# Performance work log

Measured on AMD Instinct MI355X. Metric: run time of the kernel, lower is better.

## Reference

```python
import jax, jax.numpy as jnp
import numpy as np

D_MODEL = 768
NUM_HEADS = 12
HEAD_DIM = D_MODEL // NUM_HEADS
ROPE_THETA = 10000.0
MAX_SEQ_LEN = 2048
BATCH = 2
SEQ = 2048


def _rope_tables():
    # powers = arange(0, d_k, 2)/d_k ; freqs = theta**-powers ; angles = t outer freqs
    powers = jnp.arange(0, HEAD_DIM, 2, dtype=jnp.float32) / HEAD_DIM
    freqs = 1.0 / (ROPE_THETA ** powers)                      # [d_k/2]
    t = jnp.arange(MAX_SEQ_LEN, dtype=jnp.float32)
    angles = t[:, None] * freqs[None, :]                      # [max_seq_len, d_k/2]
    return jnp.cos(angles), jnp.sin(angles)


def _apply_rope(x, cos, sin, pos):
    # x: [b, h, s, d], pos: [b, s]; interleaved even/odd pairing
    c = cos[pos][:, None]          # [b, 1, s, d/2]
    s = sin[pos][:, None]
    x_even = x[..., 0::2]
    x_odd = x[..., 1::2]
    new_even = x_even * c - x_odd * s
    new_odd = x_even * s + x_odd * c
    # re-interleave: (..., f, 2) -> (..., 2f)
    return jnp.stack([new_even, new_odd], axis=-1).reshape(x.shape)


def setup_inputs() -> dict:
    key = jax.random.key(0)
    k1, k2, k3 = jax.random.split(key, 3)
    x = jax.random.normal(k1, (BATCH, SEQ, D_MODEL), dtype=jnp.float32)
    token_positions = jnp.broadcast_to(jnp.arange(SEQ, dtype=jnp.int32), (BATCH, SEQ))
    sigma_qkv = (2.0 / (D_MODEL + 3 * D_MODEL)) ** 0.5
    sigma_o = (2.0 / (D_MODEL + D_MODEL)) ** 0.5
    W_qkv = jax.random.normal(k2, (3 * D_MODEL, D_MODEL), dtype=jnp.float32) * sigma_qkv
    W_o = jax.random.normal(k3, (D_MODEL, D_MODEL), dtype=jnp.float32) * sigma_o
    return {"x": x, "token_positions": token_positions, "W_qkv": W_qkv, "W_o": W_o}


def reference(x, token_positions, W_qkv, W_o):
    b, s, _ = x.shape
    cos, sin = _rope_tables()
    qkv = jnp.einsum('bsd,ed->bse', x, W_qkv)                 # [b, s, 3*d_model]
    qkv = qkv.reshape(b, s, 3, NUM_HEADS, HEAD_DIM)
    qkv = jnp.transpose(qkv, (2, 0, 3, 1, 4))                 # [3, b, h, s, hd]
    q, k, v = qkv[0], qkv[1], qkv[2]
    q = _apply_rope(q, cos, sin, token_positions)
    k = _apply_rope(k, cos, sin, token_positions)
    scores = jnp.einsum('bhqd,bhkd->bhqk', q, k) / (HEAD_DIM ** 0.5)
    causal = jnp.tril(jnp.ones((s, s), dtype=bool))
    scores = jnp.where(causal, scores, -jnp.inf)
    weights = jax.nn.softmax(scores, axis=-1)
    context = jnp.einsum('bhqk,bhkd->bhqd', weights, v)
    context = jnp.transpose(context, (0, 2, 1, 3)).reshape(b, s, D_MODEL)
    return jnp.einsum('bsd,ed->bse', context, W_o)
```

## Files before the change

kernel.cpp:

```cpp
#include <hip/hip_runtime.h>
#include <hip/hip_bf16.h>
#include <math.h>

#define SEQ 2048
#define DM 768
#define NH 12
#define HD 64
#define NB 2
#define NT (NB*SEQ)
#define E3 (3*DM)

using short4v = __attribute__((ext_vector_type(4))) short;
using short8v = __attribute__((ext_vector_type(8))) short;
using floatx4 = __attribute__((ext_vector_type(4))) float;
using int4v   = __attribute__((ext_vector_type(4))) int;

#if __has_builtin(__builtin_amdgcn_exp2f)
#define EXPFN(x) __builtin_amdgcn_exp2f(x)
#define QSCALE 0.1803368801111244f
#else
#define EXPFN(x) __expf(x)
#define QSCALE 0.125f
#endif

static __device__ __forceinline__ short bfb(float f) {
  union { __hip_bfloat16 h; short s; } u;
  u.h = __float2bfloat16(f);
  return u.s;
}

static __device__ __forceinline__ void gload_lds16(const __hip_bfloat16* g, __hip_bfloat16* lds) {
  __builtin_amdgcn_global_load_lds(
      (const __attribute__((address_space(1))) unsigned int*)g,
      (__attribute__((address_space(3))) unsigned int*)lds, 16, 0, 0);
}

static __device__ __forceinline__ int swzg(int row) {
  return (((row >> 3) & 3) + 2 * (row & 3)) & 7;
}

#define XN4 (NT * DM / 4)
#define WQN4 (E3 * DM / 4)
#define WON4 (DM * DM / 4)
#define CVT_N (XN4 + WQN4 + WON4)
__global__ void cvt3_rope(const float* __restrict__ x, const float* __restrict__ wq,
                          const float* __restrict__ wo,
                          __hip_bfloat16* __restrict__ xb, __hip_bfloat16* __restrict__ wqb,
                          __hip_bfloat16* __restrict__ wob, float2* __restrict__ rcs) {
  int i = blockIdx.x * blockDim.x + threadIdx.x;
  if (i >= CVT_N) {
    int idx = i - CVT_N;
    if (idx < SEQ * 32) {
      int pos = idx >> 5, j = idx & 31;
      float freq = __expf(-(float)j * (logf(10000.0f) / 32.0f));
      float ang = (float)pos * freq;
      rcs[idx] = make_float2(cosf(ang), sinf(ang));
    }
    return;
  }
  const float* src;
  __hip_bfloat16* dst;
  int k;
  if (i < XN4) { src = x; dst = xb; k = i; }
  else if (i < XN4 + WQN4) { src = wq; dst = wqb; k = i - XN4; }
  else { src = wo; dst = wob; k = i - XN4 - WQN4; }
  floatx4 v = ((const floatx4*)src)[k];
  short4v o;
  o[0] = bfb(v[0]); o[1] = bfb(v[1]); o[2] = bfb(v[2]); o[3] = bfb(v[3]);
  ((short4v*)dst)[k] = o;
}

__global__ __launch_bounds__(256) void qkv_gemm_rope(
    const __hip_bfloat16* __restrict__ Wq,
    const __hip_bfloat16* __restrict__ Xb,
    const int* __restrict__ tpos,
    const float2* __restrict__ rcs,
    __hip_bfloat16* __restrict__ Qb, __hip_bfloat16* __restrict__ Kb,
    __hip_bfloat16* __restrict__ Vt)
{
  __shared__ __align__(16) __hip_bfloat16 As[64 * 128];
  __shared__ __align__(16) __hip_bfloat16 Bs[128 * 128];
  const int tid = threadIdx.x;
  const int lane = tid & 63, w = tid >> 6;
  const int c = lane & 15, g = lane >> 4;
  const int wr = w >> 1, wc = w & 1;
  const int bid = blockIdx.x;
  const int xcd = bid & 7, i_ = bid >> 3;
  const int nb = xcd * 4 + (i_ & 3), mb = i_ >> 2;
  const int m0 = mb * 64, n0 = nb * 128;
  const int srow = tid >> 4, sslot = tid & 15;

  floatx4 acc[2][4] = {};
  for (int k0 = 0; k0 < DM; k0 += 128) {
#pragma unroll
    for (int j = 0; j < 4; ++j) {
      const int row = j * 16 + srow;
      const int gs = (sslot ^ (row & 15)) * 8;
      gload_lds16(Wq + (size_t)(m0 + row) * DM + k0 + gs, As + j * 2048 + w * 512);
    }
#pragma unroll
    for (int j = 0; j < 8; ++j) {
      const int row = j * 16 + srow;
      const int gs = (sslot ^ (row & 15)) * 8;
      gload_lds16(Xb + (size_t)(n0 + row) * DM + k0 + gs, Bs + j * 2048 + w * 512);
    }
    __syncthreads();
#pragma unroll
    for (int kk = 0; kk < 4; ++kk) {
      short8v a[2], b[4];
#pragma unroll
      for (int i = 0; i < 2; ++i) {
        const int row = wr * 32 + i * 16 + c;
        a[i] = *(const short8v*)&As[row * 128 + (((kk * 4 + g) ^ (row & 15)) * 8)];
      }
#pragma unroll
      for (int j = 0; j < 4; ++j) {
        const int row = wc * 64 + j * 16 + c;
        b[j] = *(const short8v*)&Bs[row * 128 + (((kk * 4 + g) ^ (row & 15)) * 8)];
      }
#pragma unroll
      for (int i = 0; i < 2; ++i)
#pragma unroll
        for (int j = 0; j < 4; ++j)
          acc[i][j] = __builtin_amdgcn_mfma_f32_16x16x32_bf16(a[i], b[j], acc[i][j], 0, 0, 0);
    }
    __syncthreads();
  }
#pragma unroll
  for (int i = 0; i < 2; ++i) {
    const int e0 = m0 + wr * 32 + i * 16 + 4 * g;
    const int jj = (e0 & 63) >> 1;
#pragma unroll
    for (int j = 0; j < 4; ++j) {
      const int t = n0 + wc * 64 + j * 16 + c;
      const int b_ = t >> 11, s = t & (SEQ - 1);
      float v0 = acc[i][j][0], v1 = acc[i][j][1], v2 = acc[i][j][2], v3 = acc[i][j][3];
      if (e0 < 2 * DM) {
        const int pos = tpos[t];
        const float2 cs0 = rcs[pos * 32 + jj];
        const float2 cs1 = rcs[pos * 32 + jj + 1];
        const float n0v = v0 * cs0.x - v1 * cs0.y, n1v = v0 * cs0.y + v1 * cs0.x;
        const float n2v = v2 * cs1.x - v3 * cs1.y, n3v = v2 * cs1.y + v3 * cs1.x;
        v0 = n0v; v1 = n1v; v2 = n2v; v3 = n3v;
      }
      if (e0 < DM) {
        const int h = e0 >> 6, d = e0 & 63;
        short4v pk;
        pk[0] = bfb(v0 * QSCALE); pk[1] = bfb(v1 * QSCALE);
        pk[2] = bfb(v2 * QSCALE); pk[3] = bfb(v3 * QSCALE);
        *(short4v*)&Qb[(((size_t)(b_ * NH + h) * SEQ) + s) * HD + d] = pk;
      } else if (e0 < 2 * DM) {
        const int e = e0 - DM, h = e >> 6, d = e & 63;
        short4v pk;
        pk[0] = bfb(v0); pk[1] = bfb(v1); pk[2] = bfb(v2); pk[3] = bfb(v3);
        *(short4v*)&Kb[(((size_t)(b_ * NH + h) * SEQ) + s) * HD + d] = pk;
      } else {
        const int e = e0 - 2 * DM, h = e >> 6, d = e & 63;
        const size_t base = ((size_t)(b_ * NH + h) * HD + d) * SEQ + s;
        Vt[base]           = __float2bfloat16(v0);
        Vt[base + SEQ]     = __float2bfloat16(v1);
        Vt[base + 2 * SEQ] = __float2bfloat16(v2);
        Vt[base + 3 * SEQ] = __float2bfloat16(v3);
      }
    }
  }
}

__global__ __launch_bounds__(512) void attn_fused(
    const __hip_bfloat16* __restrict__ Qb,
    const __hip_bfloat16* __restrict__ Kb,
    const __hip_bfloat16* __restrict__ Vt,
    __hip_bfloat16* __restrict__ Cx)
{
  __shared__ __align__(16) __hip_bfloat16 Ks[2][128 * 64];
  __shared__ __align__(16) __hip_bfloat16 Vs[2][64 * 128];
  const int tid = threadIdx.x;
  const int lane = tid & 63, w = tid >> 6;
  const int c = lane & 15, g = lane >> 4;
  const int bid = blockIdx.x;
  const int xcd = bid & 7, i_ = bid >> 3;
  const int bh = xcd + 8 * (i_ % 3);
  const int qG = 15 - i_ / 3;
  const int KBmax = qG;
  const __hip_bfloat16* Qh = Qb + (size_t)bh * SEQ * HD;
  const __hip_bfloat16* Kh = Kb + (size_t)bh * SEQ * HD;
  const __hip_bfloat16* Vh = Vt + (size_t)bh * HD * SEQ;
  const int q1 = qG * 128 + w * 16 + c;
  const int qt_w = 4 * qG + (w >> 1);
  const int qrl32 = (w & 1) * 16 + c;
  const short8v qf10 = *(const short8v*)&Qh[(size_t)q1 * HD + g * 8];
  const short8v qf11 = *(const short8v*)&Qh[(size_t)q1 * HD + 32 + g * 8];
  floatx4 o1[4] = {};
  float l1 = 0.0f;
  const int kr1 = 8 * (c >> 2) + (c & 3);

  const int ksr = w * 8 + (lane >> 3), kss = lane & 7;
  const int vsr = w * 4 + (lane >> 4), vss = lane & 15;

#define STAGE_KV(KB_, KSD, VSD)                                                       \
  do {                                                                               \
    _Pragma("unroll")                                                                \
    for (int j = 0; j < 2; ++j) {                                                    \
      const int kr = j * 64 + ksr;                                                   \
      gload_lds16(Kh + (size_t)((KB_) * 128 + kr) * HD + ((kss ^ swzg(kr)) * 8),     \
                  (KSD) + j * 4096 + w * 512);                                       \
      const int vr = j * 32 + vsr;                                                   \
      gload_lds16(Vh + (size_t)vr * SEQ + (KB_) * 128 + ((vss ^ (vr & 15)) * 8),     \
                  (VSD) + j * 4096 + w * 512);                                       \
    }                                                                                \
  } while (0)

  STAGE_KV(0, Ks[0], Vs[0]);
  __syncthreads();
  int cb = 0;
  for (int kb = 0; kb <= KBmax; ++kb) {
    if (kb < KBmax) STAGE_KV(kb + 1, Ks[cb ^ 1], Vs[cb ^ 1]);
    {
      const __hip_bfloat16* Kt = Ks[cb];
      const __hip_bfloat16* Vb = Vs[cb];
#pragma unroll
      for (int s = 0; s < 4; ++s) {
        const int kidx = 4 * kb + s;
        if (kidx <= qt_w) {
          const int r0 = s * 32 + kr1, r1 = r0 + 4;
          const int z0 = swzg(r0), z1 = swzg(r1);
          const short8v a00 = *(const short8v*)&Kt[r0 * 64 + ((g ^ z0) * 8)];
          const short8v a01 = *(const short8v*)&Kt[r0 * 64 + (((4 + g) ^ z0) * 8)];
          const short8v a10 = *(const short8v*)&Kt[r1 * 64 + ((g ^ z1) * 8)];
          const short8v a11 = *(const short8v*)&Kt[r1 * 64 + (((4 + g) ^ z1) * 8)];
          short8v vf[4];
#pragma unroll
          for (int f = 0; f < 4; ++f) {
            const int rv = f * 16 + c;
            vf[f] = *(const short8v*)&Vb[rv * 128 + (((s * 4 + g) ^ (rv & 15)) * 8)];
          }
          floatx4 s1a = {}, s1b = {};
          s1a = __builtin_amdgcn_mfma_f32_16x16x32_bf16(a00, qf10, s1a, 0, 0, 0);
          s1a = __builtin_amdgcn_mfma_f32_16x16x32_bf16(a01, qf11, s1a, 0, 0, 0);
          s1b = __builtin_amdgcn_mfma_f32_16x16x32_bf16(a10, qf10, s1b, 0, 0, 0);
          s1b = __builtin_amdgcn_mfma_f32_16x16x32_bf16(a11, qf11, s1b, 0, 0, 0);
          if (kidx == qt_w) {
#pragma unroll
            for (int r = 0; r < 4; ++r) {
              if (8 * g + r > qrl32) s1a[r] = -INFINITY;
              if (8 * g + r + 4 > qrl32) s1b[r] = -INFINITY;
            }
          }
          short8v pf1;
#pragma unroll
          for (int r = 0; r < 4; ++r) {
            float p;
            p = EXPFN(s1a[r]); l1 += p; pf1[r] = bfb(p);
            p = EXPFN(s1b[r]); l1 += p; pf1[r + 4] = bfb(p);
          }
          o1[0] = __builtin_amdgcn_mfma_f32_16x16x32_bf16(vf[0], pf1, o1[0], 0, 0, 0);
          o1[1] = __builtin_amdgcn_mfma_f32_16x16x32_bf16(vf[1], pf1, o1[1], 0, 0, 0);
          o1[2] = __builtin_amdgcn_mfma_f32_16x16x32_bf16(vf[2], pf1, o1[2], 0, 0, 0);
          o1[3] = __builtin_amdgcn_mfma_f32_16x16x32_bf16(vf[3], pf1, o1[3], 0, 0, 0);
        }
      }
    }
    __syncthreads();
    cb ^= 1;
  }
#undef STAGE_KV

  l1 += __shfl_xor(l1, 16); l1 += __shfl_xor(l1, 32);
  const float inv1 = 1.0f / l1;
  const int bb = bh / NH, h = bh - bb * NH;
  const size_t trow1 = ((size_t)bb * SEQ + q1) * DM + (size_t)h * HD;
#pragma unroll
  for (int f = 0; f < 4; ++f) {
    short4v pk1;
#pragma unroll
    for (int r = 0; r < 4; ++r) pk1[r] = bfb(o1[f][r] * inv1);
    *(short4v*)&Cx[trow1 + f * 16 + 4 * g] = pk1;
  }
}

__global__ __launch_bounds__(256) void out_gemm(
    const __hip_bfloat16* __restrict__ Wo,
    const __hip_bfloat16* __restrict__ Cx,
    float* __restrict__ out)
{
  __shared__ __align__(16) __hip_bfloat16 As[128 * 64];
  __shared__ __align__(16) __hip_bfloat16 Bs[128 * 64];
  const int tid = threadIdx.x;
  const int lane = tid & 63, w = tid >> 6;
  const int c = lane & 15, g = lane >> 4;
  const int wr = w >> 1, wc = w & 1;
  const int m0 = blockIdx.y * 128;
  const int n0 = blockIdx.x * 128;
  const int srow = tid >> 3, sslot = tid & 7;

  floatx4 acc[4][4] = {};
  for (int k0 = 0; k0 < DM; k0 += 64) {
#pragma unroll
    for (int j = 0; j < 4; ++j) {
      const int row = j * 32 + srow;
      const int gs = (sslot ^ (row & 7)) * 8;
      gload_lds16(Wo + (size_t)(m0 + row) * DM + k0 + gs, As + j * 2048 + w * 512);
      gload_lds16(Cx + (size_t)(n0 + row) * DM + k0 + gs, Bs + j * 2048 + w * 512);
    }
    __syncthreads();
#pragma unroll
    for (int kk = 0; kk < 2; ++kk) {
      short8v a[4], b[4];
#pragma unroll
      for (int i = 0; i < 4; ++i) {
        const int row = wr * 64 + i * 16 + c;
        a[i] = *(const short8v*)&As[row * 64 + (((kk * 4 + g) ^ (row & 7)) * 8)];
      }
#pragma unroll
      for (int j = 0; j < 4; ++j) {
        const int row = wc * 64 + j * 16 + c;
        b[j] = *(const short8v*)&Bs[row * 64 + (((kk * 4 + g) ^ (row & 7)) * 8)];
      }
#pragma unroll
      for (int i = 0; i < 4; ++i)
#pragma unroll
        for (int j = 0; j < 4; ++j)
          acc[i][j] = __builtin_amdgcn_mfma_f32_16x16x32_bf16(a[i], b[j], acc[i][j], 0, 0, 0);
    }
    __syncthreads();
  }
#pragma unroll
  for (int i = 0; i < 4; ++i) {
    const int e0 = m0 + wr * 64 + i * 16 + 4 * g;
#pragma unroll
    for (int j = 0; j < 4; ++j) {
      const int t = n0 + wc * 64 + j * 16 + c;
      *(floatx4*)&out[(size_t)t * DM + e0] = acc[i][j];
    }
  }
}

extern "C" void kernel_launch(void* const* d_in, const int* in_sizes, int n_in,
                              void* d_out, int out_size, void* d_ws, size_t ws_size,
                              hipStream_t stream) {
  const float* x    = (const float*)d_in[0];
  const int*   tpos = (const int*)d_in[1];
  const float* Wq   = (const float*)d_in[2];
  const float* Wo   = (const float*)d_in[3];
  float* out = (float*)d_out;

  const size_t QKV_BYTES = (size_t)NB * NH * SEQ * HD * 2;
  const size_t REQUIRED = 4 * QKV_BYTES;
  if (ws_size < REQUIRED) return;

  char* ws = (char*)d_ws;
  __hip_bfloat16* Qb = (__hip_bfloat16*)(ws);
  __hip_bfloat16* Kb = (__hip_bfloat16*)(ws + QKV_BYTES);
  __hip_bfloat16* Vt = (__hip_bfloat16*)(ws + 2 * QKV_BYTES);
  __hip_bfloat16* Cx = (__hip_bfloat16*)(ws + 3 * QKV_BYTES);
  __hip_bfloat16* xb = (__hip_bfloat16*)(ws + 3 * QKV_BYTES);
  char* ob = (char*)d_out;
  float2* rcs = (float2*)(ob);
  __hip_bfloat16* wqb = (__hip_bfloat16*)(ob + (size_t)SEQ * 32 * 8);
  __hip_bfloat16* wob = (__hip_bfloat16*)(ob + (size_t)SEQ * 32 * 8 + (size_t)E3 * DM * 2);

  const int TOT_N = CVT_N + SEQ * 32;
  cvt3_rope<<<dim3((TOT_N + 255) / 256), dim3(256), 0, stream>>>(x, Wq, Wo, xb, wqb, wob, rcs);
  qkv_gemm_rope<<<dim3(1152), dim3(256), 0, stream>>>(wqb, xb, tpos, rcs, Qb, Kb, Vt);
  attn_fused<<<dim3(384), dim3(512), 0, stream>>>(Qb, Kb, Vt, Cx);
  out_gemm<<<dim3(32, 6), dim3(256), 0, stream>>>(wob, Cx, out);
}
```

Measured before the change: 88.33 us.

## Add per-XCD atomic work queue to attention and retile output GEMM

The attention kernel becomes persistent: 512 blocks pull (head, query-tile) tasks from per-XCD atomic counters, which cvt3_rope zeroes first, taking the longest causal tiles first to even out load. The output projection GEMM switches to 64x128 tiles with a K-step of 128 and XCD-aware block mapping, which gives 384 blocks instead of 192 and more parallelism. The counters live in scratch space inside the output buffer. The risks are atomic and extra barrier overhead, plus a larger LDS footprint in out_gemm.

```diff
diff --git a/kernel.cpp b/kernel.cpp
--- a/kernel.cpp
+++ b/kernel.cpp
@@ -46,8 +46,10 @@
 __global__ void cvt3_rope(const float* __restrict__ x, const float* __restrict__ wq,
                           const float* __restrict__ wo,
                           __hip_bfloat16* __restrict__ xb, __hip_bfloat16* __restrict__ wqb,
-                          __hip_bfloat16* __restrict__ wob, float2* __restrict__ rcs) {
+                          __hip_bfloat16* __restrict__ wob, float2* __restrict__ rcs,
+                          int* __restrict__ qcnt) {
   int i = blockIdx.x * blockDim.x + threadIdx.x;
+  if (blockIdx.x == 0 && threadIdx.x < 8) qcnt[threadIdx.x] = 0;
   if (i >= CVT_N) {
     int idx = i - CVT_N;
     if (idx < SEQ * 32) {
@@ -170,111 +172,118 @@
     const __hip_bfloat16* __restrict__ Qb,
     const __hip_bfloat16* __restrict__ Kb,
     const __hip_bfloat16* __restrict__ Vt,
-    __hip_bfloat16* __restrict__ Cx)
+    __hip_bfloat16* __restrict__ Cx,
+    int* __restrict__ qcnt)
 {
   __shared__ __align__(16) __hip_bfloat16 Ks[2][128 * 64];
   __shared__ __align__(16) __hip_bfloat16 Vs[2][64 * 128];
+  __shared__ int task_s;
   const int tid = threadIdx.x;
   const int lane = tid & 63, w = tid >> 6;
   const int c = lane & 15, g = lane >> 4;
-  const int bid = blockIdx.x;
-  const int xcd = bid & 7, i_ = bid >> 3;
-  const int bh = xcd + 8 * (i_ % 3);
-  const int qG = 15 - i_ / 3;
-  const int KBmax = qG;
-  const __hip_bfloat16* Qh = Qb + (size_t)bh * SEQ * HD;
-  const __hip_bfloat16* Kh = Kb + (size_t)bh * SEQ * HD;
-  const __hip_bfloat16* Vh = Vt + (size_t)bh * HD * SEQ;
-  const int q1 = qG * 128 + w * 16 + c;
-  const int qt_w = 4 * qG + (w >> 1);
-  const int qrl32 = (w & 1) * 16 + c;
-  const short8v qf10 = *(const short8v*)&Qh[(size_t)q1 * HD + g * 8];
-  const short8v qf11 = *(const short8v*)&Qh[(size_t)q1 * HD + 32 + g * 8];
-  floatx4 o1[4] = {};
-  float l1 = 0.0f;
+  const int xcd = blockIdx.x & 7;
   const int kr1 = 8 * (c >> 2) + (c & 3);
-
   const int ksr = w * 8 + (lane >> 3), kss = lane & 7;
   const int vsr = w * 4 + (lane >> 4), vss = lane & 15;
 
-#define STAGE_KV(KB_, KSD, VSD)                                                       \
-  do {                                                                               \
-    _Pragma("unroll")                                                                \
-    for (int j = 0; j < 2; ++j) {                                                    \
-      const int kr = j * 64 + ksr;                                                   \
-      gload_lds16(Kh + (size_t)((KB_) * 128 + kr) * HD + ((kss ^ swzg(kr)) * 8),     \
-                  (KSD) + j * 4096 + w * 512);                                       \
-      const int vr = j * 32 + vsr;                                                   \
-      gload_lds16(Vh + (size_t)vr * SEQ + (KB_) * 128 + ((vss ^ (vr & 15)) * 8),     \
-                  (VSD) + j * 4096 + w * 512);                                       \
-    }                                                                                \
-  } while (0)
-
-  STAGE_KV(0, Ks[0], Vs[0]);
-  __syncthreads();
-  int cb = 0;
-  for (int kb = 0; kb <= KBmax; ++kb) {
-    if (kb < KBmax) STAGE_KV(kb + 1, Ks[cb ^ 1], Vs[cb ^ 1]);
-    {
-      const __hip_bfloat16* Kt = Ks[cb];
-      const __hip_bfloat16* Vb = Vs[cb];
-#pragma unroll
-      for (int s = 0; s < 4; ++s) {
-        const int kidx = 4 * kb + s;
-        if (kidx <= qt_w) {
-          const int r0 = s * 32 + kr1, r1 = r0 + 4;
-          const int z0 = swzg(r0), z1 = swzg(r1);
-          const short8v a00 = *(const short8v*)&Kt[r0 * 64 + ((g ^ z0) * 8)];
-          const short8v a01 = *(const short8v*)&Kt[r0 * 64 + (((4 + g) ^ z0) * 8)];
-          const short8v a10 = *(const short8v*)&Kt[r1 * 64 + ((g ^ z1) * 8)];
-          const short8v a11 = *(const short8v*)&Kt[r1 * 64 + (((4 + g) ^ z1) * 8)];
-          short8v vf[4];
-#pragma unroll
-          for (int f = 0; f < 4; ++f) {
-            const int rv = f * 16 + c;
-            vf[f] = *(const short8v*)&Vb[rv * 128 + (((s * 4 + g) ^ (rv & 15)) * 8)];
+  for (;;) {
+    if (tid == 0) task_s = atomicAdd(&qcnt[xcd], 1);
+    __syncthreads();
+    const int task = task_s;
+    if (task >= 48) return;
+    const int qG = 15 - task / 3;
+    const int bh = xcd + 8 * (task % 3);
+    const int KBmax = qG;
+    const __hip_bfloat16* Qh = Qb + (size_t)bh * SEQ * HD;
+    const __hip_bfloat16* Kh = Kb + (size_t)bh * SEQ * HD;
+    const __hip_bfloat16* Vh = Vt + (size_t)bh * HD * SEQ;
+    const int q1 = qG * 128 + w * 16 + c;
+    const int qt_w = 4 * qG + (w >> 1);
+    const int qrl32 = (w & 1) * 16 + c;
+    const short8v qf10 = *(const short8v*)&Qh[(size_t)q1 * HD + g * 8];
+    const short8v qf11 = *(const short8v*)&Qh[(size_t)q1 * HD + 32 + g * 8];
+    floatx4 o1[4] = {};
+    float l1 = 0.0f;
+
+#define STAGE_KV(KB_, KSD, VSD)                                                      \
+    do {                                                                             \
+      _Pragma("unroll")                                                              \
+      for (int j = 0; j < 2; ++j) {                                                  \
+        const int kr = j * 64 + ksr;                                                 \
+        gload_lds16(Kh + (size_t)((KB_) * 128 + kr) * HD + ((kss ^ swzg(kr)) * 8),   \
+                    (KSD) + j * 4096 + w * 512);                                     \
+        const int vr = j * 32 + vsr;                                                 \
+        gload_lds16(Vh + (size_t)vr * SEQ + (KB_) * 128 + ((vss ^ (vr & 15)) * 8),   \
+                    (VSD) + j * 4096 + w * 512);                                     \
+      }                                                                              \
+    } while (0)
+
+    STAGE_KV(0, Ks[0], Vs[0]);
+    __syncthreads();
+    int cb = 0;
+    for (int kb = 0; kb <= KBmax; ++kb) {
+      if (kb < KBmax) STAGE_KV(kb + 1, Ks[cb ^ 1], Vs[cb ^ 1]);
+      {
+        const __hip_bfloat16* Kt = Ks[cb];
+        const __hip_bfloat16* Vb = Vs[cb];
+#pragma unroll
+        for (int s = 0; s < 4; ++s) {
+          const int kidx = 4 * kb + s;
+          if (kidx <= qt_w) {
+            const int r0 = s * 32 + kr1, r1 = r0 + 4;
+            const int z0 = swzg(r0), z1 = swzg(r1);
+            const short8v a00 = *(const short8v*)&Kt[r0 * 64 + ((g ^ z0) * 8)];
+            const short8v a01 = *(const short8v*)&Kt[r0 * 64 + (((4 + g) ^ z0) * 8)];
+            const short8v a10 = *(const short8v*)&Kt[r1 * 64 + ((g ^ z1) * 8)];
+            const short8v a11 = *(const short8v*)&Kt[r1 * 64 + (((4 + g) ^ z1) * 8)];
+            short8v vf[4];
+#pragma unroll
+            for (int f = 0; f < 4; ++f) {
+              const int rv = f * 16 + c;
+              vf[f] = *(const short8v*)&Vb[rv * 128 + (((s * 4 + g) ^ (rv & 15)) * 8)];
+            }
+            floatx4 s1a = {}, s1b = {};
+            s1a = __builtin_amdgcn_mfma_f32_16x16x32_bf16(a00, qf10, s1a, 0, 0, 0);
+            s1a = __builtin_amdgcn_mfma_f32_16x16x32_bf16(a01, qf11, s1a, 0, 0, 0);
+            s1b = __builtin_amdgcn_mfma_f32_16x16x32_bf16(a10, qf10, s1b, 0, 0, 0);
+            s1b = __builtin_amdgcn_mfma_f32_16x16x32_bf16(a11, qf11, s1b, 0, 0, 0);
+            if (kidx == qt_w) {
+#pragma unroll
+              for (int r = 0; r < 4; ++r) {
+                if (8 * g + r > qrl32) s1a[r] = -INFINITY;
+                if (8 * g + r + 4 > qrl32) s1b[r] = -INFINITY;
+              }
+            }
+            short8v pf1;
+#pragma unroll
+            for (int r = 0; r < 4; ++r) {
+              float p;
+              p = EXPFN(s1a[r]); l1 += p; pf1[r] = bfb(p);
+              p = EXPFN(s1b[r]); l1 += p; pf1[r + 4] = bfb(p);
+            }
+            o1[0] = __builtin_amdgcn_mfma_f32_16x16x32_bf16(vf[0], pf1, o1[0], 0, 0, 0);
+            o1[1] = __builtin_amdgcn_mfma_f32_16x16x32_bf16(vf[1], pf1, o1[1], 0, 0, 0);
+            o1[2] = __builtin_amdgcn_mfma_f32_16x16x32_bf16(vf[2], pf1, o1[2], 0, 0, 0);
+            o1[3] = __builtin_amdgcn_mfma_f32_16x16x32_bf16(vf[3], pf1, o1[3], 0, 0, 0);
           }
-          floatx4 s1a = {}, s1b = {};
-          s1a = __builtin_amdgcn_mfma_f32_16x16x32_bf16(a00, qf10, s1a, 0, 0, 0);
-          s1a = __builtin_amdgcn_mfma_f32_16x16x32_bf16(a01, qf11, s1a, 0, 0, 0);
-          s1b = __builtin_amdgcn_mfma_f32_16x16x32_bf16(a10, qf10, s1b, 0, 0, 0);
-          s1b = __builtin_amdgcn_mfma_f32_16x16x32_bf16(a11, qf11, s1b, 0, 0, 0);
-          if (kidx == qt_w) {
-#pragma unroll
-            for (int r = 0; r < 4; ++r) {
-              if (8 * g + r > qrl32) s1a[r] = -INFINITY;
-              if (8 * g + r + 4 > qrl32) s1b[r] = -INFINITY;
-            }
-          }
-          short8v pf1;
-#pragma unroll
-          for (int r = 0; r < 4; ++r) {
-            float p;
-            p = EXPFN(s1a[r]); l1 += p; pf1[r] = bfb(p);
-            p = EXPFN(s1b[r]); l1 += p; pf1[r + 4] = bfb(p);
-          }
-          o1[0] = __builtin_amdgcn_mfma_f32_16x16x32_bf16(vf[0], pf1, o1[0], 0, 0, 0);
-          o1[1] = __builtin_amdgcn_mfma_f32_16x16x32_bf16(vf[1], pf1, o1[1], 0, 0, 0);
-          o1[2] = __builtin_amdgcn_mfma_f32_16x16x32_bf16(vf[2], pf1, o1[2], 0, 0, 0);
-          o1[3] = __builtin_amdgcn_mfma_f32_16x16x32_bf16(vf[3], pf1, o1[3], 0, 0, 0);
         }
       }
-    }
-    __syncthreads();
-    cb ^= 1;
-  }
+      __syncthreads();
+      cb ^= 1;
+    }
 #undef STAGE_KV
 
-  l1 += __shfl_xor(l1, 16); l1 += __shfl_xor(l1, 32);
-  const float inv1 = 1.0f / l1;
-  const int bb = bh / NH, h = bh - bb * NH;
-  const size_t trow1 = ((size_t)bb * SEQ + q1) * DM + (size_t)h * HD;
-#pragma unroll
-  for (int f = 0; f < 4; ++f) {
-    short4v pk1;
-#pragma unroll
-    for (int r = 0; r < 4; ++r) pk1[r] = bfb(o1[f][r] * inv1);
-    *(short4v*)&Cx[trow1 + f * 16 + 4 * g] = pk1;
+    l1 += __shfl_xor(l1, 16); l1 += __shfl_xor(l1, 32);
+    const float inv1 = 1.0f / l1;
+    const int bb = bh / NH, h = bh - bb * NH;
+    const size_t trow1 = ((size_t)bb * SEQ + q1) * DM + (size_t)h * HD;
+#pragma unroll
+    for (int f = 0; f < 4; ++f) {
+      short4v pk1;
+#pragma unroll
+      for (int r = 0; r < 4; ++r) pk1[r] = bfb(o1[f][r] * inv1);
+      *(short4v*)&Cx[trow1 + f * 16 + 4 * g] = pk1;
+    }
   }
 }
 
@@ -283,41 +292,48 @@
     const __hip_bfloat16* __restrict__ Cx,
     float* __restrict__ out)
 {
-  __shared__ __align__(16) __hip_bfloat16 As[128 * 64];
-  __shared__ __align__(16) __hip_bfloat16 Bs[128 * 64];
+  __shared__ __align__(16) __hip_bfloat16 As[64 * 128];
+  __shared__ __align__(16) __hip_bfloat16 Bs[128 * 128];
   const int tid = threadIdx.x;
   const int lane = tid & 63, w = tid >> 6;
   const int c = lane & 15, g = lane >> 4;
   const int wr = w >> 1, wc = w & 1;
-  const int m0 = blockIdx.y * 128;
-  const int n0 = blockIdx.x * 128;
-  const int srow = tid >> 3, sslot = tid & 7;
-
-  floatx4 acc[4][4] = {};
-  for (int k0 = 0; k0 < DM; k0 += 64) {
+  const int bid = blockIdx.x;
+  const int xcd = bid & 7, i_ = bid >> 3;
+  const int nb = xcd * 4 + (i_ & 3), mb = i_ >> 2;
+  const int m0 = mb * 64, n0 = nb * 128;
+  const int srow = tid >> 4, sslot = tid & 15;
+
+  floatx4 acc[2][4] = {};
+  for (int k0 = 0; k0 < DM; k0 += 128) {
 #pragma unroll
     for (int j = 0; j < 4; ++j) {
-      const int row = j * 32 + srow;
-      const int gs = (sslot ^ (row & 7)) * 8;
+      const int row = j * 16 + srow;
+      const int gs = (sslot ^ (row & 15)) * 8;
       gload_lds16(Wo + (size_t)(m0 + row) * DM + k0 + gs, As + j * 2048 + w * 512);
+    }
+#pragma unroll
+    for (int j = 0; j < 8; ++j) {
+      const int row = j * 16 + srow;
+      const int gs = (sslot ^ (row & 15)) * 8;
       gload_lds16(Cx + (size_t)(n0 + row) * DM + k0 + gs, Bs + j * 2048 + w * 512);
     }
     __syncthreads();
 #pragma unroll
-    for (int kk = 0; kk < 2; ++kk) {
-      short8v a[4], b[4];
-#pragma unroll
-      for (int i = 0; i < 4; ++i) {
-        const int row = wr * 64 + i * 16 + c;
-        a[i] = *(const short8v*)&As[row * 64 + (((kk * 4 + g) ^ (row & 7)) * 8)];
+    for (int kk = 0; kk < 4; ++kk) {
+      short8v a[2], b[4];
+#pragma unroll
+      for (int i = 0; i < 2; ++i) {
+        const int row = wr * 32 + i * 16 + c;
+        a[i] = *(const short8v*)&As[row * 128 + (((kk * 4 + g) ^ (row & 15)) * 8)];
       }
 #pragma unroll
       for (int j = 0; j < 4; ++j) {
         const int row = wc * 64 + j * 16 + c;
-        b[j] = *(const short8v*)&Bs[row * 64 + (((kk * 4 + g) ^ (row & 7)) * 8)];
-      }
-#pragma unroll
-      for (int i = 0; i < 4; ++i)
+        b[j] = *(const short8v*)&Bs[row * 128 + (((kk * 4 + g) ^ (row & 15)) * 8)];
+      }
+#pragma unroll
+      for (int i = 0; i < 2; ++i)
 #pragma unroll
         for (int j = 0; j < 4; ++j)
           acc[i][j] = __builtin_amdgcn_mfma_f32_16x16x32_bf16(a[i], b[j], acc[i][j], 0, 0, 0);
@@ -325,8 +341,8 @@
     __syncthreads();
   }
 #pragma unroll
-  for (int i = 0; i < 4; ++i) {
-    const int e0 = m0 + wr * 64 + i * 16 + 4 * g;
+  for (int i = 0; i < 2; ++i) {
+    const int e0 = m0 + wr * 32 + i * 16 + 4 * g;
 #pragma unroll
     for (int j = 0; j < 4; ++j) {
       const int t = n0 + wc * 64 + j * 16 + c;
@@ -358,10 +374,11 @@
   float2* rcs = (float2*)(ob);
   __hip_bfloat16* wqb = (__hip_bfloat16*)(ob + (size_t)SEQ * 32 * 8);
   __hip_bfloat16* wob = (__hip_bfloat16*)(ob + (size_t)SEQ * 32 * 8 + (size_t)E3 * DM * 2);
+  int* qcnt = (int*)(ob + (size_t)SEQ * 32 * 8 + (size_t)E3 * DM * 2 + (size_t)DM * DM * 2);
 
   const int TOT_N = CVT_N + SEQ * 32;
-  cvt3_rope<<<dim3((TOT_N + 255) / 256), dim3(256), 0, stream>>>(x, Wq, Wo, xb, wqb, wob, rcs);
+  cvt3_rope<<<dim3((TOT_N + 255) / 256), dim3(256), 0, stream>>>(x, Wq, Wo, xb, wqb, wob, rcs, qcnt);
   qkv_gemm_rope<<<dim3(1152), dim3(256), 0, stream>>>(wqb, xb, tpos, rcs, Qb, Kb, Vt);
-  attn_fused<<<dim3(384), dim3(512), 0, stream>>>(Qb, Kb, Vt, Cx);
-  out_gemm<<<dim3(32, 6), dim3(256), 0, stream>>>(wob, Cx, out);
-}
+  attn_fused<<<dim3(512), dim3(512), 0, stream>>>(Qb, Kb, Vt, Cx, qcnt);
+  out_gemm<<<dim3(384), dim3(256), 0, stream>>>(wob, Cx, out);
+}
```

Result: no change. 87.19 us (-1.3%).
